# Performance work log

Measured on AMD Instinct MI355X. Metric: run time of the kernel, lower is better.

## Reference

```python
import jax, jax.numpy as jnp
import numpy as np

Q_PTS = jnp.array([0.0, 0.25, 0.5, 0.75, 1.0], dtype=jnp.float32)
LN_EPS = 1e-5


def _lower_median(s):
    # torch.median returns the LOWER of the two middle values for even n
    return s[..., (s.shape[-1] - 1) // 2]


def _quantile_sorted(s, q):
    # torch.quantile default 'linear' interpolation, computed on pre-sorted s
    n = s.shape[-1]
    idx = q * (n - 1)
    lo = jnp.floor(idx).astype(jnp.int32)
    hi = jnp.ceil(idx).astype(jnp.int32)
    frac = (idx - lo).astype(s.dtype)
    return jnp.take(s, lo, axis=-1) * (1.0 - frac) + jnp.take(s, hi, axis=-1) * frac


def _robust_stats(flat):
    # flat: [L-1, B, N] -> [L-1, B, 7]  (median, MAD, 5 quantiles)
    s = jnp.sort(flat, axis=-1)
    med = _lower_median(s)[..., None]
    mad = _lower_median(jnp.sort(jnp.abs(flat - med), axis=-1))[..., None]
    q = _quantile_sorted(s, Q_PTS)
    return jnp.concatenate([med, mad, q], axis=-1)


def _layer_norm(x, eps=LN_EPS):
    mu = x.mean(-1, keepdims=True)
    var = ((x - mu) ** 2).mean(-1, keepdims=True)
    return (x - mu) * jax.lax.rsqrt(var + eps)


def _forward(ws, bs, fc1_w, fc1_b, ln_w, ln_b, gate_w, gate_b, fco_w, fco_b, scale):
    Lm1, B = ws.shape[0], ws.shape[1]
    w_flat = ws.reshape(Lm1, B, -1)
    b_flat = bs.reshape(Lm1, B, -1)
    w_feats = _robust_stats(w_flat)            # [L-1, B, 7]
    b_feats = _robust_stats(b_flat)            # [L-1, B, 7]
    g_mean = w_flat.mean(-1, keepdims=True)    # [L-1, B, 1]
    g_mad = jnp.zeros_like(g_mean)             # MAD over a size-1 axis is exactly 0
    combined = jnp.concatenate([w_feats, b_feats, g_mean, g_mad], axis=-1)  # [L-1, B, 16]
    x = _layer_norm(combined)                  # F.layer_norm without affine
    # ResidualMLP (vectorized over the layer axis l)
    h = jnp.einsum('lbi,lhi->lbh', x, fc1_w) + fc1_b[:, None, :]
    h = _layer_norm(h) * ln_w[:, None, :] + ln_b[:, None, :]
    h = jax.nn.gelu(h, approximate=False)      # nn.GELU() default = exact erf
    gate = jax.nn.sigmoid(jnp.einsum('lbh,lgh->lbg', h, gate_w) + gate_b[:, None, :])
    raw = jnp.einsum('lbg,log->lbo', h * gate, fco_w) + fco_b[:, None, :]
    return jnp.sin(raw) * scale[:, None, None] + 1.0   # [L-1, B, out_dim]


def setup_inputs() -> dict:
    key = jax.random.key(0)
    ks = jax.random.split(key, 8)
    Lm1, B, D, H, F_IN = 3, 64, 512, 64, 16
    return {
        'ws': jax.random.normal(ks[0], (Lm1, B, D, D), jnp.float32) * 0.05,
        'bs': jax.random.normal(ks[1], (Lm1, B, D), jnp.float32) * 0.05,
        'w_last': jax.random.normal(ks[2], (B, D, D), jnp.float32) * 0.05,
        'b_last': jax.random.normal(ks[3], (B, D), jnp.float32) * 0.05,
        'fc1_w': jax.random.normal(ks[4], (Lm1, H, F_IN), jnp.float32) * 0.2,
        'fc1_b': jnp.zeros((Lm1, H), jnp.float32),
        'ln_w': jnp.ones((Lm1, H), jnp.float32),
        'ln_b': jnp.zeros((Lm1, H), jnp.float32),
        'gate_w': jax.random.normal(ks[5], (Lm1, H, H), jnp.float32) * 0.15,
        'gate_b': jnp.zeros((Lm1, H), jnp.float32),
        'fco_w': jax.random.normal(ks[6], (Lm1, D, H), jnp.float32) * 0.1,
        'fco_b': jnp.zeros((Lm1, D), jnp.float32),
        'scale': jnp.full((Lm1,), 0.1, jnp.float32),
    }


def reference(ws, bs, w_last, b_last, fc1_w, fc1_b, ln_w, ln_b, gate_w, gate_b, fco_w, fco_b, scale):
    # w_last / b_last correspond to wsfeat[L-1]: received by forward but never used
    # (loop breaks at i == L-1), matching the torch module exactly.
    return _forward(ws, bs, fc1_w, fc1_b, ln_w, ln_b, gate_w, gate_b, fco_w, fco_b, scale)
```

## Files before the change

kernel.cpp:

```cpp
#include <hip/hip_runtime.h>
#include <cstdint>

#define NROW 192
#define NW   262144
#define NW4  65536
#define NT   1024
#define QCAP 1024
#define MCAP 6144

__device__ __forceinline__ uint32_t mono(float x) {
    uint32_t u = __float_as_uint(x);
    return (u & 0x80000000u) ? ~u : (u | 0x80000000u);
}
__device__ __forceinline__ float unmono(uint32_t u) {
    uint32_t v = (u & 0x80000000u) ? (u & 0x7FFFFFFFu) : ~u;
    return __uint_as_float(v);
}
__device__ __forceinline__ int binof(float x, float lo, float s) {
    float d = (x - lo) * s;
    d = fminf(fmaxf(d, 0.0f), 4095.0f);
    return (int)d;
}

__device__ void block_select(const uint32_t* hist, int nb, uint32_t rank,
                             uint32_t* sbuf, volatile uint32_t* out, int tid) {
    int per = (nb + NT - 1) / NT;
    int base = tid * per;
    uint32_t s = 0;
    for (int i = 0; i < per; ++i) { int idx = base + i; if (idx < nb) s += hist[idx]; }
    uint32_t p = s;
    int lane = tid & 63;
    #pragma unroll
    for (int off = 1; off < 64; off <<= 1) {
        uint32_t v = __shfl_up(p, off);
        if (lane >= off) p += v;
    }
    int w = tid >> 6;
    if (lane == 63) sbuf[w] = p;
    __syncthreads();
    if (tid == 0) {
        uint32_t acc = 0;
        for (int i = 0; i < 16; ++i) { uint32_t t = sbuf[i]; sbuf[16 + i] = acc; acc += t; }
    }
    __syncthreads();
    uint32_t excl = sbuf[16 + w] + p - s;
    if (rank >= excl && rank < excl + s) {
        uint32_t rem = rank - excl;
        for (int i = 0; i < per; ++i) {
            int idx = base + i;
            if (idx >= nb) break;
            uint32_t c = hist[idx];
            if (rem < c) { out[0] = (uint32_t)idx; out[1] = rem; break; }
            rem -= c;
        }
    }
    __syncthreads();
}

__device__ uint32_t seg_select(const uint32_t* seg, uint32_t cnt, uint32_t rank,
                               uint32_t* hist2, uint32_t* sbuf,
                               volatile uint32_t* out2, int tid) {
    for (int i = tid; i < 2048; i += NT) hist2[i] = 0;
    __syncthreads();
    for (uint32_t i = tid; i < cnt; i += NT) atomicAdd(&hist2[seg[i] >> 21], 1u);
    __syncthreads();
    block_select(hist2, 2048, rank, sbuf, out2, tid);
    uint32_t b1 = out2[0], r1 = out2[1];
    __syncthreads();
    for (int i = tid; i < 2048; i += NT) hist2[i] = 0;
    __syncthreads();
    for (uint32_t i = tid; i < cnt; i += NT) {
        uint32_t k = seg[i];
        if ((k >> 21) == b1) atomicAdd(&hist2[(k >> 10) & 2047u], 1u);
    }
    __syncthreads();
    block_select(hist2, 2048, r1, sbuf, out2, tid);
    uint32_t b2 = out2[0], r2 = out2[1];
    __syncthreads();
    for (int i = tid; i < 1024; i += NT) hist2[i] = 0;
    __syncthreads();
    for (uint32_t i = tid; i < cnt; i += NT) {
        uint32_t k = seg[i];
        if ((k >> 21) == b1 && ((k >> 10) & 2047u) == b2)
            atomicAdd(&hist2[k & 1023u], 1u);
    }
    __syncthreads();
    block_select(hist2, 1024, r2, sbuf, out2, tid);
    uint32_t b3 = out2[0];
    __syncthreads();
    return (b1 << 21) + (b2 << 10) + b3;
}

__device__ uint32_t refine_global(const float4* p4, float med, int mode,
                                  uint32_t b1, uint32_t rem,
                                  uint32_t* hist2, uint32_t* sbuf,
                                  volatile uint32_t* out2, int tid) {
    for (int i = tid; i < 2048; i += NT) hist2[i] = 0;
    __syncthreads();
    for (int it = 0; it < 64; ++it) {
        float4 v = p4[tid + it * NT];
        float xs[4] = {v.x, v.y, v.z, v.w};
        #pragma unroll
        for (int c = 0; c < 4; ++c) {
            uint32_t u = mode ? __float_as_uint(fabsf(xs[c] - med)) : mono(xs[c]);
            if ((u >> 20) == b1) atomicAdd(&hist2[(u >> 9) & 2047u], 1u);
        }
    }
    __syncthreads();
    block_select(hist2, 2048, rem, sbuf, out2, tid);
    uint32_t b2 = out2[0], r2 = out2[1];
    __syncthreads();
    for (int i = tid; i < 512; i += NT) hist2[i] = 0;
    __syncthreads();
    for (int it = 0; it < 64; ++it) {
        float4 v = p4[tid + it * NT];
        float xs[4] = {v.x, v.y, v.z, v.w};
        #pragma unroll
        for (int c = 0; c < 4; ++c) {
            uint32_t u = mode ? __float_as_uint(fabsf(xs[c] - med)) : mono(xs[c]);
            if ((u >> 20) == b1 && ((u >> 9) & 2047u) == b2)
                atomicAdd(&hist2[u & 511u], 1u);
        }
    }
    __syncthreads();
    block_select(hist2, 512, r2, sbuf, out2, tid);
    uint32_t b3 = out2[0];
    __syncthreads();
    return (b1 << 20) + (b2 << 9) + b3;
}

__device__ void fb_path(const float4* p4, float* feat, int row,
                        uint32_t* hist, uint32_t* hist2, uint32_t* sbuf,
                        volatile uint32_t* out2, int tid) {
    const uint32_t RANK6[6] = {65535u, 65536u, 131071u, 131072u, 196607u, 196608u};
    for (int i = tid; i < 4096; i += NT) hist[i] = 0;
    __syncthreads();
    for (int it = 0; it < 64; ++it) {
        float4 v = p4[tid + it * NT];
        float xs[4] = {v.x, v.y, v.z, v.w};
        #pragma unroll
        for (int c = 0; c < 4; ++c) atomicAdd(&hist[mono(xs[c]) >> 20], 1u);
    }
    __syncthreads();
    uint32_t bins[6], rems[6];
    for (int k = 0; k < 6; ++k) {
        block_select(hist, 4096, RANK6[k], sbuf, out2, tid);
        bins[k] = out2[0]; rems[k] = out2[1];
        __syncthreads();
    }
    float svv[6];
    for (int k = 0; k < 6; ++k)
        svv[k] = unmono(refine_global(p4, 0.f, 0, bins[k], rems[k], hist2, sbuf, out2, tid));
    if (tid == 0) {
        float* f = feat + row * 16;
        f[0] = svv[2];
        f[3] = 0.25f * svv[0] + 0.75f * svv[1];
        f[4] = 0.5f  * (svv[2] + svv[3]);
        f[5] = 0.75f * svv[4] + 0.25f * svv[5];
    }
    float med = svv[2];
    __syncthreads();
    for (int i = tid; i < 4096; i += NT) hist[i] = 0;
    __syncthreads();
    for (int it = 0; it < 64; ++it) {
        float4 v = p4[tid + it * NT];
        float xs[4] = {v.x, v.y, v.z, v.w};
        #pragma unroll
        for (int c = 0; c < 4; ++c)
            atomicAdd(&hist[__float_as_uint(fabsf(xs[c] - med)) >> 20], 1u);
    }
    __syncthreads();
    block_select(hist, 4096, 131071u, sbuf, out2, tid);
    uint32_t mb = out2[0], mr = out2[1];
    __syncthreads();
    uint32_t mu = refine_global(p4, med, 1, mb, mr, hist2, sbuf, out2, tid);
    if (tid == 0) feat[row * 16 + 1] = __uint_as_float(mu);
}

__global__ __launch_bounds__(NT) void wstats_kernel(const float* __restrict__ wsrc,
                                                    float* __restrict__ feat) {
    const int row = blockIdx.x;
    const int tid = threadIdx.x;
    const float4* __restrict__ p4 = (const float4*)(wsrc + (size_t)row * NW);

    __shared__ uint32_t hist[4096];
    __shared__ uint32_t hist2[2048];
    __shared__ uint32_t sbuf[1024];
    __shared__ uint32_t segs[MCAP];
    __shared__ uint32_t ctrl[48];
    __shared__ float fctrl[8];
    volatile uint32_t* out2 = (volatile uint32_t*)(ctrl + 40);

    const int lane = tid & 63, w = tid >> 6;
    float* fsb = (float*)sbuf;

    {
        float smin = 1e30f, smax = -1e30f;
        #pragma unroll
        for (int k = 0; k < 8; ++k) {
            float4 v = p4[tid + k * NT];
            smin = fminf(smin, fminf(fminf(v.x, v.y), fminf(v.z, v.w)));
            smax = fmaxf(smax, fmaxf(fmaxf(v.x, v.y), fmaxf(v.z, v.w)));
        }
        #pragma unroll
        for (int off = 32; off > 0; off >>= 1) {
            smin = fminf(smin, __shfl_down(smin, off));
            smax = fmaxf(smax, __shfl_down(smax, off));
        }
        if (lane == 0) { fsb[w * 2] = smin; fsb[w * 2 + 1] = smax; }
        __syncthreads();
        if (tid == 0) {
            float mn = 1e30f, mx = -1e30f;
            for (int i = 0; i < 16; ++i) { mn = fminf(mn, fsb[i * 2]); mx = fmaxf(mx, fsb[i * 2 + 1]); }
            float span = mx - mn;
            float lo = mn - 0.0625f * span;
            float s = (span > 0.f) ? 4096.0f / (span * 1.125f) : 0.0f;
            fctrl[0] = lo; fctrl[1] = s;
        }
        __syncthreads();
    }
    const float blo = fctrl[0], bsc = fctrl[1];

    for (int i = tid; i < 4096; i += NT) hist[i] = 0;
    __syncthreads();
    {
        float sum = 0.f, fmn = 1e30f, fmx = -1e30f;
        for (int it = 0; it < 64; it += 8) {
            float4 a[8];
            #pragma unroll
            for (int j = 0; j < 8; ++j) a[j] = p4[tid + (it + j) * NT];
            #pragma unroll
            for (int j = 0; j < 8; ++j) {
                float xs[4] = {a[j].x, a[j].y, a[j].z, a[j].w};
                #pragma unroll
                for (int c = 0; c < 4; ++c) {
                    float x = xs[c];
                    sum += x;
                    fmn = fminf(fmn, x);
                    fmx = fmaxf(fmx, x);
                    atomicAdd(&hist[binof(x, blo, bsc)], 1u);
                }
            }
        }
        #pragma unroll
        for (int off = 32; off > 0; off >>= 1) {
            sum += __shfl_down(sum, off);
            fmn = fminf(fmn, __shfl_down(fmn, off));
            fmx = fmaxf(fmx, __shfl_down(fmx, off));
        }
        __syncthreads();
        if (lane == 0) { fsb[w * 4] = sum; fsb[w * 4 + 1] = fmn; fsb[w * 4 + 2] = fmx; }
        __syncthreads();
        if (tid == 0) { float s = 0; for (int i = 0; i < 16; ++i) s += fsb[i * 4]; feat[row * 16 + 14] = s * (1.0f / (float)NW); }
        if (tid == 1) { float m = 1e30f;  for (int i = 0; i < 16; ++i) m = fminf(m, fsb[i * 4 + 1]); feat[row * 16 + 2] = m; fctrl[2] = m; }
        if (tid == 2) { float M = -1e30f; for (int i = 0; i < 16; ++i) M = fmaxf(M, fsb[i * 4 + 2]); feat[row * 16 + 6] = M; fctrl[3] = M; }
        if (tid == 3) feat[row * 16 + 15] = 0.0f;
        __syncthreads();
    }

    const uint32_t RANKS[6] = {65535u, 65536u, 131071u, 131072u, 196607u, 196608u};
    for (int k = 0; k < 6; ++k) {
        block_select(hist, 4096, RANKS[k], sbuf, out2, tid);
        if (tid == 0) { ctrl[12 + k] = out2[0]; ctrl[18 + k] = out2[1]; }
        __syncthreads();
    }
    if (tid == 0) {
        uint32_t nd = 0;
        for (int k = 0; k < 6; ++k) {
            uint32_t b = ctrl[12 + k];
            int j = -1;
            for (uint32_t t = 0; t < nd; ++t) if (ctrl[24 + t] == b) { j = (int)t; break; }
            if (j < 0) { j = (int)nd; ctrl[24 + nd] = b; nd++; }
            ctrl[32 + k] = (uint32_t)j;
        }
        ctrl[10] = nd; ctrl[11] = 0;
        for (int j = 0; j < 6; ++j) ctrl[j] = 0;
    }
    __syncthreads();
    const uint32_t nd = ctrl[10];
    sbuf[tid] = 0; sbuf[tid + (4096 - NT) ? 0 : 0] = sbuf[tid];
    __syncthreads();
    if (tid < (int)nd) ((uint8_t*)sbuf)[ctrl[24 + tid]] = (uint8_t)(tid + 1);
    __syncthreads();

    {
        const uint8_t* tbl = (const uint8_t*)sbuf;
        for (int it = 0; it < 64; it += 8) {
            float4 a[8];
            #pragma unroll
            for (int j = 0; j < 8; ++j) a[j] = p4[tid + (it + j) * NT];
            #pragma unroll
            for (int j = 0; j < 8; ++j) {
                float xs[4] = {a[j].x, a[j].y, a[j].z, a[j].w};
                #pragma unroll
                for (int c = 0; c < 4; ++c) {
                    float x = xs[c];
                    uint32_t m = tbl[binof(x, blo, bsc)];
                    if (m) {
                        uint32_t jj = m - 1;
                        uint32_t pos = atomicAdd(&ctrl[jj], 1u);
                        if (pos < QCAP) segs[jj * QCAP + pos] = mono(x);
                    }
                }
            }
        }
    }
    __syncthreads();
    if (tid == 0) {
        uint32_t fail = 0;
        for (uint32_t j = 0; j < nd; ++j)
            if (ctrl[j] > QCAP || ctrl[j] != hist[ctrl[24 + j]]) fail = 1;
        ctrl[11] = fail;
    }
    __syncthreads();
    if (ctrl[11]) { fb_path(p4, feat, row, hist, hist2, sbuf, out2, tid); return; }

    float sv[6];
    for (int k = 0; k < 6; ++k) {
        uint32_t j = ctrl[32 + k];
        sv[k] = unmono(seg_select(segs + j * QCAP, ctrl[j], ctrl[18 + k],
                                  hist2, sbuf, out2, tid));
    }
    const float med = sv[2];
    if (tid == 0) {
        float* f = feat + row * 16;
        f[0] = med;
        f[3] = 0.25f * sv[0] + 0.75f * sv[1];
        f[4] = 0.5f  * (sv[2] + sv[3]);
        f[5] = 0.75f * sv[4] + 0.25f * sv[5];
    }

    const float tmax = fmaxf(fctrl[3] - med, med - fctrl[2]);
    const float tsc = (tmax > 0.f) ? 4096.0f / tmax : 0.0f;
    for (int i = tid; i < 4096; i += NT) hist[i] = 0;
    __syncthreads();
    for (int it = 0; it < 64; it += 8) {
        float4 a[8];
        #pragma unroll
        for (int j = 0; j < 8; ++j) a[j] = p4[tid + (it + j) * NT];
        #pragma unroll
        for (int j = 0; j < 8; ++j) {
            float xs[4] = {a[j].x, a[j].y, a[j].z, a[j].w};
            #pragma unroll
            for (int c = 0; c < 4; ++c)
                atomicAdd(&hist[binof(fabsf(xs[c] - med), 0.0f, tsc)], 1u);
        }
    }
    __syncthreads();
    block_select(hist, 4096, 131071u, sbuf, out2, tid);
    const uint32_t mbin = out2[0], mrem = out2[1];
    if (tid == 0) ctrl[8] = 0;
    __syncthreads();

    for (int it = 0; it < 64; it += 8) {
        float4 a[8];
        #pragma unroll
        for (int j = 0; j < 8; ++j) a[j] = p4[tid + (it + j) * NT];
        #pragma unroll
        for (int j = 0; j < 8; ++j) {
            float xs[4] = {a[j].x, a[j].y, a[j].z, a[j].w};
            #pragma unroll
            for (int c = 0; c < 4; ++c) {
                float t = fabsf(xs[c] - med);
                if (binof(t, 0.0f, tsc) == (int)mbin) {
                    uint32_t pos = atomicAdd(&ctrl[8], 1u);
                    if (pos < MCAP) segs[pos] = __float_as_uint(t);
                }
            }
        }
    }
    __syncthreads();
    if (tid == 0) ctrl[11] = (ctrl[8] > MCAP || ctrl[8] != hist[mbin]) ? 1u : 0u;
    __syncthreads();
    if (ctrl[11]) { fb_path(p4, feat, row, hist, hist2, sbuf, out2, tid); return; }
    uint32_t madu = seg_select(segs, ctrl[8], mrem, hist2, sbuf, out2, tid);
    if (tid == 0) feat[row * 16 + 1] = __uint_as_float(madu);
}

__device__ void bitonic512(float* a, int tid) {
    for (int k = 2; k <= 512; k <<= 1) {
        for (int j = k >> 1; j > 0; j >>= 1) {
            __syncthreads();
            for (int i = tid; i < 512; i += 256) {
                int ixj = i ^ j;
                if (ixj > i) {
                    float x = a[i], y = a[ixj];
                    bool up = ((i & k) == 0);
                    if ((x > y) == up) { a[i] = y; a[ixj] = x; }
                }
            }
        }
    }
    __syncthreads();
}

__global__ __launch_bounds__(256) void tail_kernel(
    const float* __restrict__ bsrc, const float* __restrict__ feat,
    const float* __restrict__ fc1_w, const float* __restrict__ fc1_b,
    const float* __restrict__ ln_w,  const float* __restrict__ ln_b,
    const float* __restrict__ gate_w, const float* __restrict__ gate_b,
    const float* __restrict__ fco_w,  const float* __restrict__ fco_b,
    const float* __restrict__ scale,  float* __restrict__ out) {
    const int row = blockIdx.x;
    const int tid = threadIdx.x;
    const int l = row >> 6;
    __shared__ float a[512], d[512];
    __shared__ float x[16], h[64], hg[64], stats[2];

    if (tid < 7)       x[tid] = feat[row * 16 + tid];
    else if (tid == 7) x[14]  = feat[row * 16 + 14];
    else if (tid == 8) x[15]  = 0.0f;

    const float* p = bsrc + (size_t)row * 512;
    for (int i = tid; i < 512; i += 256) a[i] = p[i];
    bitonic512(a, tid);
    const float bmed = a[255];
    if (tid == 0) {
        x[7]  = bmed;
        x[9]  = a[0];
        x[10] = 0.25f * a[127] + 0.75f * a[128];
        x[11] = 0.5f  * (a[255] + a[256]);
        x[12] = 0.75f * a[383] + 0.25f * a[384];
        x[13] = a[511];
    }
    __syncthreads();
    for (int i = tid; i < 512; i += 256) d[i] = fabsf(a[i] - bmed);
    bitonic512(d, tid);
    if (tid == 0) x[8] = d[255];
    __syncthreads();

    if (tid == 0) {
        float mu = 0.f;
        for (int i = 0; i < 16; ++i) mu += x[i];
        mu *= (1.f / 16.f);
        float var = 0.f;
        for (int i = 0; i < 16; ++i) { float dd = x[i] - mu; var += dd * dd; }
        var *= (1.f / 16.f);
        stats[0] = mu; stats[1] = rsqrtf(var + 1e-5f);
    }
    __syncthreads();
    if (tid < 16) x[tid] = (x[tid] - stats[0]) * stats[1];
    __syncthreads();
    if (tid < 64) {
        const float* wv = fc1_w + ((size_t)l * 64 + tid) * 16;
        float acc = fc1_b[l * 64 + tid];
        #pragma unroll
        for (int i = 0; i < 16; ++i) acc += x[i] * wv[i];
        h[tid] = acc;
    }
    __syncthreads();
    if (tid == 0) {
        float mu = 0.f;
        for (int i = 0; i < 64; ++i) mu += h[i];
        mu *= (1.f / 64.f);
        float var = 0.f;
        for (int i = 0; i < 64; ++i) { float dd = h[i] - mu; var += dd * dd; }
        var *= (1.f / 64.f);
        stats[0] = mu; stats[1] = rsqrtf(var + 1e-5f);
    }
    __syncthreads();
    if (tid < 64) {
        float v = (h[tid] - stats[0]) * stats[1] * ln_w[l * 64 + tid] + ln_b[l * 64 + tid];
        h[tid] = 0.5f * v * (1.0f + erff(v * 0.70710678118654752f));
    }
    __syncthreads();
    if (tid < 64) {
        const float* wv = gate_w + ((size_t)l * 64 + tid) * 64;
        float acc = gate_b[l * 64 + tid];
        #pragma unroll
        for (int i = 0; i < 64; ++i) acc += h[i] * wv[i];
        float g = 1.0f / (1.0f + expf(-acc));
        hg[tid] = h[tid] * g;
    }
    __syncthreads();
    const float sc = scale[l];
    for (int o = tid; o < 512; o += 256) {
        const float* wv = fco_w + ((size_t)l * 512 + o) * 64;
        float acc = fco_b[l * 512 + o];
        #pragma unroll
        for (int i = 0; i < 64; ++i) acc += hg[i] * wv[i];
        out[(size_t)row * 512 + o] = sinf(acc) * sc + 1.0f;
    }
}

extern "C" void kernel_launch(void* const* d_in, const int* in_sizes, int n_in,
                              void* d_out, int out_size, void* d_ws, size_t ws_size,
                              hipStream_t stream) {
    const float* ws_in  = (const float*)d_in[0];
    const float* bs_in  = (const float*)d_in[1];
    const float* fc1_w  = (const float*)d_in[4];
    const float* fc1_b  = (const float*)d_in[5];
    const float* ln_w   = (const float*)d_in[6];
    const float* ln_b   = (const float*)d_in[7];
    const float* gate_w = (const float*)d_in[8];
    const float* gate_b = (const float*)d_in[9];
    const float* fco_w  = (const float*)d_in[10];
    const float* fco_b  = (const float*)d_in[11];
    const float* scale  = (const float*)d_in[12];
    float* out  = (float*)d_out;
    float* feat = (float*)d_ws;

    hipLaunchKernelGGL(wstats_kernel, dim3(NROW), dim3(NT), 0, stream, ws_in, feat);
    hipLaunchKernelGGL(tail_kernel, dim3(NROW), dim3(256), 0, stream,
                       bs_in, feat, fc1_w, fc1_b, ln_w, ln_b, gate_w, gate_b,
                       fco_w, fco_b, scale, out);
}
```

Measured before the change: 459.2 us.

## Predict MAD window from histogram to fuse passes and merge bias stats

Computes prefix sums of the coarse histogram so all six quantile bins are found in a single scan. The histogram is also used to bound the MAD bracket around the median before the median is known, so quantile candidates and MAD candidates are gathered in one shared data pass. This removes the separate MAD histogram and collection passes over the 1 MB rows. Exact selection inside each candidate segment now uses brute-force rank counting instead of three-level radix histograms. The bias-vector sorts move out of the MLP kernel into extra blocks of the stats kernel. The cost is O(n²) rank counting on candidate sets and several new failure checks that fall back to the slow path.

```diff
diff --git a/kernel.cpp b/kernel.cpp
--- a/kernel.cpp
+++ b/kernel.cpp
@@ -3,10 +3,9 @@
 
 #define NROW 192
 #define NW   262144
-#define NW4  65536
 #define NT   1024
 #define QCAP 1024
-#define MCAP 6144
+#define SEGS_CAP 8192
 
 __device__ __forceinline__ uint32_t mono(float x) {
     uint32_t u = __float_as_uint(x);
@@ -57,40 +56,6 @@
     __syncthreads();
 }
 
-__device__ uint32_t seg_select(const uint32_t* seg, uint32_t cnt, uint32_t rank,
-                               uint32_t* hist2, uint32_t* sbuf,
-                               volatile uint32_t* out2, int tid) {
-    for (int i = tid; i < 2048; i += NT) hist2[i] = 0;
-    __syncthreads();
-    for (uint32_t i = tid; i < cnt; i += NT) atomicAdd(&hist2[seg[i] >> 21], 1u);
-    __syncthreads();
-    block_select(hist2, 2048, rank, sbuf, out2, tid);
-    uint32_t b1 = out2[0], r1 = out2[1];
-    __syncthreads();
-    for (int i = tid; i < 2048; i += NT) hist2[i] = 0;
-    __syncthreads();
-    for (uint32_t i = tid; i < cnt; i += NT) {
-        uint32_t k = seg[i];
-        if ((k >> 21) == b1) atomicAdd(&hist2[(k >> 10) & 2047u], 1u);
-    }
-    __syncthreads();
-    block_select(hist2, 2048, r1, sbuf, out2, tid);
-    uint32_t b2 = out2[0], r2 = out2[1];
-    __syncthreads();
-    for (int i = tid; i < 1024; i += NT) hist2[i] = 0;
-    __syncthreads();
-    for (uint32_t i = tid; i < cnt; i += NT) {
-        uint32_t k = seg[i];
-        if ((k >> 21) == b1 && ((k >> 10) & 2047u) == b2)
-            atomicAdd(&hist2[k & 1023u], 1u);
-    }
-    __syncthreads();
-    block_select(hist2, 1024, r2, sbuf, out2, tid);
-    uint32_t b3 = out2[0];
-    __syncthreads();
-    return (b1 << 21) + (b2 << 10) + b3;
-}
-
 __device__ uint32_t refine_global(const float4* p4, float med, int mode,
                                   uint32_t b1, uint32_t rem,
                                   uint32_t* hist2, uint32_t* sbuf,
@@ -177,22 +142,81 @@
     if (tid == 0) feat[row * 16 + 1] = __uint_as_float(mu);
 }
 
-__global__ __launch_bounds__(NT) void wstats_kernel(const float* __restrict__ wsrc,
-                                                    float* __restrict__ feat) {
+__device__ __forceinline__ uint32_t Pv(const uint32_t* P, int k) {
+    return (k >= 4096) ? (uint32_t)NW : P[k];
+}
+__device__ __forceinline__ uint32_t wup(float mL, float mR, float tau,
+                                        float blo, float bsc, const uint32_t* P) {
+    const int bR = binof(mR + tau, blo, bsc);
+    const int bL = binof(mL - tau, blo, bsc);
+    return Pv(P, bR + 1) - P[bL];
+}
+__device__ __forceinline__ uint32_t wlow(float mL, float mR, float tau,
+                                         float blo, float bsc, const uint32_t* P) {
+    const int bR = binof(mL + tau, blo, bsc);
+    const int bL = binof(mR - tau, blo, bsc);
+    const uint32_t a = P[bR];
+    const uint32_t b = Pv(P, bL + 1);
+    return (a > b) ? (a - b) : 0u;
+}
+
+__device__ void bitonic512g(float* a, int t2) {
+    for (int k = 2; k <= 512; k <<= 1) {
+        for (int j = k >> 1; j > 0; j >>= 1) {
+            __syncthreads();
+            for (int i = t2; i < 512; i += 256) {
+                int ixj = i ^ j;
+                if (ixj > i) {
+                    float x = a[i], y = a[ixj];
+                    bool up = ((i & k) == 0);
+                    if ((x > y) == up) { a[i] = y; a[ixj] = x; }
+                }
+            }
+        }
+    }
+    __syncthreads();
+}
+
+__global__ __launch_bounds__(NT) void stats_kernel(const float* __restrict__ wsrc,
+                                                   const float* __restrict__ bsrc,
+                                                   float* __restrict__ feat) {
+    const int tid = threadIdx.x;
+    __shared__ uint32_t hist[4096];
+    __shared__ uint32_t sbuf[1024];
+    __shared__ uint32_t segs[SEGS_CAP];
+    __shared__ uint32_t ctrl[64];
+    __shared__ float fctrl[8];
+
+    if (blockIdx.x >= NROW) {
+        const int g = tid >> 8, t2 = tid & 255;
+        const int brow = (blockIdx.x - NROW) * 4 + g;
+        float* a = ((float*)segs) + g * 512;
+        float* d = ((float*)segs) + 2048 + g * 512;
+        const float* p = bsrc + (size_t)brow * 512;
+        for (int i = t2; i < 512; i += 256) a[i] = p[i];
+        bitonic512g(a, t2);
+        const float bmed = a[255];
+        if (t2 == 0) {
+            float* f = feat + brow * 16;
+            f[7]  = bmed;
+            f[9]  = a[0];
+            f[10] = 0.25f * a[127] + 0.75f * a[128];
+            f[11] = 0.5f  * (a[255] + a[256]);
+            f[12] = 0.75f * a[383] + 0.25f * a[384];
+            f[13] = a[511];
+        }
+        __syncthreads();
+        for (int i = t2; i < 512; i += 256) d[i] = fabsf(a[i] - bmed);
+        bitonic512g(d, t2);
+        if (t2 == 0) feat[brow * 16 + 8] = d[255];
+        return;
+    }
+
     const int row = blockIdx.x;
-    const int tid = threadIdx.x;
     const float4* __restrict__ p4 = (const float4*)(wsrc + (size_t)row * NW);
-
-    __shared__ uint32_t hist[4096];
-    __shared__ uint32_t hist2[2048];
-    __shared__ uint32_t sbuf[1024];
-    __shared__ uint32_t segs[MCAP];
-    __shared__ uint32_t ctrl[48];
-    __shared__ float fctrl[8];
-    volatile uint32_t* out2 = (volatile uint32_t*)(ctrl + 40);
-
-    const int lane = tid & 63, w = tid >> 6;
+    const int lane = tid & 63, wv = tid >> 6;
     float* fsb = (float*)sbuf;
+    volatile uint32_t* out2 = (volatile uint32_t*)(ctrl + 62);
 
     {
         float smin = 1e30f, smax = -1e30f;
@@ -207,7 +231,7 @@
             smin = fminf(smin, __shfl_down(smin, off));
             smax = fmaxf(smax, __shfl_down(smax, off));
         }
-        if (lane == 0) { fsb[w * 2] = smin; fsb[w * 2 + 1] = smax; }
+        if (lane == 0) { fsb[wv * 2] = smin; fsb[wv * 2 + 1] = smax; }
         __syncthreads();
         if (tid == 0) {
             float mn = 1e30f, mx = -1e30f;
@@ -226,12 +250,12 @@
     {
         float sum = 0.f, fmn = 1e30f, fmx = -1e30f;
         for (int it = 0; it < 64; it += 8) {
-            float4 a[8];
+            float4 a8[8];
             #pragma unroll
-            for (int j = 0; j < 8; ++j) a[j] = p4[tid + (it + j) * NT];
+            for (int j = 0; j < 8; ++j) a8[j] = p4[tid + (it + j) * NT];
             #pragma unroll
             for (int j = 0; j < 8; ++j) {
-                float xs[4] = {a[j].x, a[j].y, a[j].z, a[j].w};
+                float xs[4] = {a8[j].x, a8[j].y, a8[j].z, a8[j].w};
                 #pragma unroll
                 for (int c = 0; c < 4; ++c) {
                     float x = xs[c];
@@ -249,7 +273,7 @@
             fmx = fmaxf(fmx, __shfl_down(fmx, off));
         }
         __syncthreads();
-        if (lane == 0) { fsb[w * 4] = sum; fsb[w * 4 + 1] = fmn; fsb[w * 4 + 2] = fmx; }
+        if (lane == 0) { fsb[wv * 4] = sum; fsb[wv * 4 + 1] = fmn; fsb[wv * 4 + 2] = fmx; }
         __syncthreads();
         if (tid == 0) { float s = 0; for (int i = 0; i < 16; ++i) s += fsb[i * 4]; feat[row * 16 + 14] = s * (1.0f / (float)NW); }
         if (tid == 1) { float m = 1e30f;  for (int i = 0; i < 16; ++i) m = fminf(m, fsb[i * 4 + 1]); feat[row * 16 + 2] = m; fctrl[2] = m; }
@@ -258,144 +282,249 @@
         __syncthreads();
     }
 
-    const uint32_t RANKS[6] = {65535u, 65536u, 131071u, 131072u, 196607u, 196608u};
-    for (int k = 0; k < 6; ++k) {
-        block_select(hist, 4096, RANKS[k], sbuf, out2, tid);
-        if (tid == 0) { ctrl[12 + k] = out2[0]; ctrl[18 + k] = out2[1]; }
-        __syncthreads();
-    }
-    if (tid == 0) {
-        uint32_t nd = 0;
-        for (int k = 0; k < 6; ++k) {
-            uint32_t b = ctrl[12 + k];
-            int j = -1;
-            for (uint32_t t = 0; t < nd; ++t) if (ctrl[24 + t] == b) { j = (int)t; break; }
-            if (j < 0) { j = (int)nd; ctrl[24 + nd] = b; nd++; }
-            ctrl[32 + k] = (uint32_t)j;
-        }
-        ctrl[10] = nd; ctrl[11] = 0;
+    {
+        const int b4 = tid * 4;
+        const uint32_t v0 = hist[b4], v1 = hist[b4 + 1], v2 = hist[b4 + 2], v3 = hist[b4 + 3];
+        const uint32_t s = v0 + v1 + v2 + v3;
+        uint32_t p = s;
+        #pragma unroll
+        for (int off = 1; off < 64; off <<= 1) {
+            uint32_t t = __shfl_up(p, off);
+            if (lane >= off) p += t;
+        }
+        if (lane == 63) sbuf[wv] = p;
+        __syncthreads();
+        if (tid == 0) {
+            uint32_t acc = 0;
+            for (int i = 0; i < 16; ++i) { uint32_t t = sbuf[i]; sbuf[16 + i] = acc; acc += t; }
+        }
+        __syncthreads();
+        const uint32_t excl = sbuf[16 + wv] + p - s;
+        uint32_t ppA[5];
+        ppA[0] = excl; ppA[1] = excl + v0; ppA[2] = ppA[1] + v1; ppA[3] = ppA[2] + v2; ppA[4] = ppA[3] + v3;
+        hist[b4] = ppA[0]; hist[b4 + 1] = ppA[1]; hist[b4 + 2] = ppA[2]; hist[b4 + 3] = ppA[3];
+        const uint32_t RANKS[6] = {65535u, 65536u, 131071u, 131072u, 196607u, 196608u};
+        #pragma unroll
+        for (int c = 0; c < 4; ++c) {
+            #pragma unroll
+            for (int q = 0; q < 6; ++q) {
+                const uint32_t r = RANKS[q];
+                if (ppA[c] <= r && r < ppA[c + 1]) {
+                    ctrl[12 + q] = (uint32_t)(b4 + c);
+                    ctrl[18 + q] = r - ppA[c];
+                    ctrl[48 + q] = ppA[c + 1] - ppA[c];
+                }
+            }
+        }
+        __syncthreads();
+    }
+
+    if (tid == 0) {
+        uint32_t ndl = 0, fail = 0;
+        #pragma unroll
+        for (int q = 0; q < 6; ++q) {
+            const uint32_t b = ctrl[12 + q];
+            int jf = -1;
+            for (uint32_t t = 0; t < ndl; ++t) if (ctrl[24 + t] == b) { jf = (int)t; break; }
+            if (jf < 0) {
+                jf = (int)ndl;
+                ctrl[24 + ndl] = b;
+                ctrl[30 + ndl] = ctrl[48 + q];
+                ndl++;
+            }
+            ctrl[36 + q] = (uint32_t)jf;
+        }
+        uint32_t off = 0;
+        for (uint32_t t = 0; t < ndl; ++t) {
+            ctrl[54 + t] = off;
+            if (ctrl[30 + t] > QCAP) fail = 1;
+            off += ctrl[30 + t];
+        }
+        if (off > 6144u) fail = 1;
+        if (ctrl[14] == 0u || ctrl[14] == 4095u) fail = 1;
+        ctrl[60] = off;
+        ctrl[10] = ndl;
+        ctrl[11] = fail;
+        #pragma unroll
         for (int j = 0; j < 6; ++j) ctrl[j] = 0;
-    }
-    __syncthreads();
-    const uint32_t nd = ctrl[10];
-    sbuf[tid] = 0; sbuf[tid + (4096 - NT) ? 0 : 0] = sbuf[tid];
-    __syncthreads();
-    if (tid < (int)nd) ((uint8_t*)sbuf)[ctrl[24 + tid]] = (uint8_t)(tid + 1);
-    __syncthreads();
-
+        ctrl[6] = 0;
+        ctrl[7] = 0;
+        ctrl[8] = 0;
+        ctrl[9] = 0;
+        ctrl[48] = 0xFFFFFFFFu; ctrl[49] = 0xFFFFFFFFu;
+    }
+    __syncthreads();
+    if (ctrl[11]) { fb_path(p4, feat, row, hist, segs, sbuf, out2, tid); return; }
+
+    const float wbin = 1.0f / bsc;
+    const uint32_t m0 = ctrl[14];
+
+    sbuf[tid] = 0;
+    {
+        const float mLf = blo + (float)m0 * wbin;
+        const float mRf = mLf + wbin;
+        #pragma unroll
+        for (int c = 0; c < 4; ++c) {
+            const int j = tid * 4 + c;
+            const float tau = (float)j * wbin;
+            const uint32_t up_j = wup(mLf, mRf, tau, blo, bsc, hist);
+            if (up_j <= 131071u) {
+                bool bnd = (j == 4095);
+                if (!bnd) bnd = (wup(mLf, mRf, (float)(j + 1) * wbin, blo, bsc, hist) > 131071u);
+                if (bnd) ctrl[48] = (uint32_t)j;
+            }
+            const uint32_t lo_j = wlow(mLf, mRf, tau, blo, bsc, hist);
+            if (lo_j >= 131072u) {
+                bool bnd = (j == 0);
+                if (!bnd) bnd = (wlow(mLf, mRf, (float)(j - 1) * wbin, blo, bsc, hist) < 131072u);
+                if (bnd) ctrl[49] = (uint32_t)j;
+            }
+        }
+    }
+    __syncthreads();
+    if (tid < (int)ctrl[10]) ((uint8_t*)sbuf)[ctrl[24 + tid]] = (uint8_t)(tid + 1);
+    const uint32_t jlo = ctrl[48], jhi = ctrl[49];
+    float Awin = (jlo == 0xFFFFFFFFu) ? -1.0f : (float)jlo * wbin;
+    float Bwin = (jhi == 0xFFFFFFFFu) ? 3.0e38f : (float)jhi * wbin;
+    Bwin = fmaxf(Bwin, Awin + 3.0f * wbin);
+    const float mtld = blo + ((float)m0 + 0.5f) * wbin;
+    const uint32_t madbase = ctrl[60];
+    __syncthreads();
+
+    uint32_t myclo = 0;
     {
         const uint8_t* tbl = (const uint8_t*)sbuf;
         for (int it = 0; it < 64; it += 8) {
-            float4 a[8];
+            float4 a8[8];
             #pragma unroll
-            for (int j = 0; j < 8; ++j) a[j] = p4[tid + (it + j) * NT];
+            for (int j = 0; j < 8; ++j) a8[j] = p4[tid + (it + j) * NT];
             #pragma unroll
             for (int j = 0; j < 8; ++j) {
-                float xs[4] = {a[j].x, a[j].y, a[j].z, a[j].w};
+                float xs[4] = {a8[j].x, a8[j].y, a8[j].z, a8[j].w};
                 #pragma unroll
                 for (int c = 0; c < 4; ++c) {
                     float x = xs[c];
                     uint32_t m = tbl[binof(x, blo, bsc)];
                     if (m) {
-                        uint32_t jj = m - 1;
+                        uint32_t jj = m - 1u;
                         uint32_t pos = atomicAdd(&ctrl[jj], 1u);
-                        if (pos < QCAP) segs[jj * QCAP + pos] = mono(x);
+                        if (pos < ctrl[30 + jj]) segs[ctrl[54 + jj] + pos] = mono(x);
+                    }
+                    float u = fabsf(x - mtld);
+                    if (u <= Awin) myclo++;
+                    else if (u <= Bwin) {
+                        uint32_t pos = atomicAdd(&ctrl[6], 1u);
+                        uint32_t slot = madbase + pos;
+                        if (slot < SEGS_CAP) segs[slot] = __float_as_uint(x);
                     }
                 }
             }
         }
     }
     __syncthreads();
-    if (tid == 0) {
+    #pragma unroll
+    for (int off = 32; off > 0; off >>= 1) myclo += __shfl_down(myclo, off);
+    if (lane == 0) sbuf[wv] = myclo;
+    __syncthreads();
+    if (tid == 0) {
+        uint32_t clo = 0;
+        for (int i = 0; i < 16; ++i) clo += sbuf[i];
+        ctrl[7] = clo;
         uint32_t fail = 0;
-        for (uint32_t j = 0; j < nd; ++j)
-            if (ctrl[j] > QCAP || ctrl[j] != hist[ctrl[24 + j]]) fail = 1;
+        const uint32_t ndl = ctrl[10];
+        for (uint32_t j = 0; j < ndl; ++j) if (ctrl[j] != ctrl[30 + j]) fail = 1;
+        if (ctrl[6] > SEGS_CAP - madbase) fail = 1;
         ctrl[11] = fail;
     }
     __syncthreads();
-    if (ctrl[11]) { fb_path(p4, feat, row, hist, hist2, sbuf, out2, tid); return; }
-
-    float sv[6];
-    for (int k = 0; k < 6; ++k) {
-        uint32_t j = ctrl[32 + k];
-        sv[k] = unmono(seg_select(segs + j * QCAP, ctrl[j], ctrl[18 + k],
-                                  hist2, sbuf, out2, tid));
-    }
-    const float med = sv[2];
+    if (ctrl[11]) { fb_path(p4, feat, row, hist, segs, sbuf, out2, tid); return; }
+
+    {
+        const uint32_t ndl = ctrl[10];
+        for (uint32_t j = 0; j < ndl; ++j) {
+            const uint32_t cnt = ctrl[j];
+            const uint32_t base = ctrl[54 + j];
+            if ((uint32_t)tid < cnt) {
+                const uint32_t key = segs[base + tid];
+                uint32_t r = 0;
+                for (uint32_t i = 0; i < cnt; ++i) {
+                    const uint32_t ki = segs[base + i];
+                    r += (ki < key || (ki == key && i < (uint32_t)tid)) ? 1u : 0u;
+                }
+                #pragma unroll
+                for (int q = 0; q < 6; ++q)
+                    if (ctrl[36 + q] == j && ctrl[18 + q] == r) ctrl[42 + q] = key;
+            }
+        }
+    }
+    __syncthreads();
+    const float med = unmono(ctrl[44]);
     if (tid == 0) {
         float* f = feat + row * 16;
         f[0] = med;
-        f[3] = 0.25f * sv[0] + 0.75f * sv[1];
-        f[4] = 0.5f  * (sv[2] + sv[3]);
-        f[5] = 0.75f * sv[4] + 0.25f * sv[5];
-    }
-
-    const float tmax = fmaxf(fctrl[3] - med, med - fctrl[2]);
-    const float tsc = (tmax > 0.f) ? 4096.0f / tmax : 0.0f;
-    for (int i = tid; i < 4096; i += NT) hist[i] = 0;
-    __syncthreads();
-    for (int it = 0; it < 64; it += 8) {
-        float4 a[8];
-        #pragma unroll
-        for (int j = 0; j < 8; ++j) a[j] = p4[tid + (it + j) * NT];
-        #pragma unroll
-        for (int j = 0; j < 8; ++j) {
-            float xs[4] = {a[j].x, a[j].y, a[j].z, a[j].w};
+        f[3] = 0.25f * unmono(ctrl[42]) + 0.75f * unmono(ctrl[43]);
+        f[4] = 0.5f  * (med + unmono(ctrl[45]));
+        f[5] = 0.75f * unmono(ctrl[46]) + 0.25f * unmono(ctrl[47]);
+    }
+
+    const uint32_t mcnt = ctrl[6];
+    const float thq = Awin + wbin;
+    const float tcq = Bwin - 2.0f * wbin;
+    float tk[8];
+    uint32_t rr[8];
+    uint32_t n2t = 0, n2c = 0;
+    #pragma unroll
+    for (int q = 0; q < 8; ++q) {
+        const uint32_t i = (uint32_t)tid + (uint32_t)q * NT;
+        float t = 3.0e38f;
+        if (i < mcnt) {
+            float x = __uint_as_float(segs[madbase + i]);
+            t = fabsf(x - med);
+            segs[madbase + i] = __float_as_uint(t);
+            n2t += (t <= thq) ? 1u : 0u;
+            n2c += (t <= tcq) ? 1u : 0u;
+        }
+        tk[q] = t;
+        rr[q] = 0;
+    }
+    #pragma unroll
+    for (int off = 32; off > 0; off >>= 1) {
+        n2t += __shfl_down(n2t, off);
+        n2c += __shfl_down(n2c, off);
+    }
+    if (lane == 0) { atomicAdd(&ctrl[8], n2t); atomicAdd(&ctrl[9], n2c); }
+    __syncthreads();
+    if (tid == 0) {
+        const uint32_t clo = ctrl[7];
+        uint32_t fail = 0;
+        if (clo > 131071u) fail = 1;
+        if (clo + ctrl[8] > 131071u) fail = 1;
+        if (clo + ctrl[9] < 131072u) fail = 1;
+        if (!fail && (131071u - clo) >= mcnt) fail = 1;
+        ctrl[11] = fail;
+    }
+    __syncthreads();
+    if (ctrl[11]) { fb_path(p4, feat, row, hist, segs, sbuf, out2, tid); return; }
+    const uint32_t kR = 131071u - ctrl[7];
+    if ((uint32_t)tid < mcnt) {
+        for (uint32_t jj = 0; jj < mcnt; ++jj) {
+            const float tj = __uint_as_float(segs[madbase + jj]);
             #pragma unroll
-            for (int c = 0; c < 4; ++c)
-                atomicAdd(&hist[binof(fabsf(xs[c] - med), 0.0f, tsc)], 1u);
-        }
-    }
-    __syncthreads();
-    block_select(hist, 4096, 131071u, sbuf, out2, tid);
-    const uint32_t mbin = out2[0], mrem = out2[1];
-    if (tid == 0) ctrl[8] = 0;
-    __syncthreads();
-
-    for (int it = 0; it < 64; it += 8) {
-        float4 a[8];
-        #pragma unroll
-        for (int j = 0; j < 8; ++j) a[j] = p4[tid + (it + j) * NT];
-        #pragma unroll
-        for (int j = 0; j < 8; ++j) {
-            float xs[4] = {a[j].x, a[j].y, a[j].z, a[j].w};
-            #pragma unroll
-            for (int c = 0; c < 4; ++c) {
-                float t = fabsf(xs[c] - med);
-                if (binof(t, 0.0f, tsc) == (int)mbin) {
-                    uint32_t pos = atomicAdd(&ctrl[8], 1u);
-                    if (pos < MCAP) segs[pos] = __float_as_uint(t);
-                }
-            }
-        }
-    }
-    __syncthreads();
-    if (tid == 0) ctrl[11] = (ctrl[8] > MCAP || ctrl[8] != hist[mbin]) ? 1u : 0u;
-    __syncthreads();
-    if (ctrl[11]) { fb_path(p4, feat, row, hist, hist2, sbuf, out2, tid); return; }
-    uint32_t madu = seg_select(segs, ctrl[8], mrem, hist2, sbuf, out2, tid);
-    if (tid == 0) feat[row * 16 + 1] = __uint_as_float(madu);
-}
-
-__device__ void bitonic512(float* a, int tid) {
-    for (int k = 2; k <= 512; k <<= 1) {
-        for (int j = k >> 1; j > 0; j >>= 1) {
-            __syncthreads();
-            for (int i = tid; i < 512; i += 256) {
-                int ixj = i ^ j;
-                if (ixj > i) {
-                    float x = a[i], y = a[ixj];
-                    bool up = ((i & k) == 0);
-                    if ((x > y) == up) { a[i] = y; a[ixj] = x; }
-                }
-            }
-        }
-    }
-    __syncthreads();
-}
-
-__global__ __launch_bounds__(256) void tail_kernel(
-    const float* __restrict__ bsrc, const float* __restrict__ feat,
+            for (int q = 0; q < 8; ++q) {
+                const uint32_t idx = (uint32_t)tid + (uint32_t)q * NT;
+                rr[q] += (tj < tk[q] || (tj == tk[q] && jj < idx)) ? 1u : 0u;
+            }
+        }
+        #pragma unroll
+        for (int q = 0; q < 8; ++q) {
+            const uint32_t idx = (uint32_t)tid + (uint32_t)q * NT;
+            if (idx < mcnt && rr[q] == kR) feat[row * 16 + 1] = tk[q];
+        }
+    }
+}
+
+__global__ __launch_bounds__(256) void mlp_kernel(
+    const float* __restrict__ feat,
     const float* __restrict__ fc1_w, const float* __restrict__ fc1_b,
     const float* __restrict__ ln_w,  const float* __restrict__ ln_b,
     const float* __restrict__ gate_w, const float* __restrict__ gate_b,
@@ -404,29 +533,9 @@
     const int row = blockIdx.x;
     const int tid = threadIdx.x;
     const int l = row >> 6;
-    __shared__ float a[512], d[512];
     __shared__ float x[16], h[64], hg[64], stats[2];
 
-    if (tid < 7)       x[tid] = feat[row * 16 + tid];
-    else if (tid == 7) x[14]  = feat[row * 16 + 14];
-    else if (tid == 8) x[15]  = 0.0f;
-
-    const float* p = bsrc + (size_t)row * 512;
-    for (int i = tid; i < 512; i += 256) a[i] = p[i];
-    bitonic512(a, tid);
-    const float bmed = a[255];
-    if (tid == 0) {
-        x[7]  = bmed;
-        x[9]  = a[0];
-        x[10] = 0.25f * a[127] + 0.75f * a[128];
-        x[11] = 0.5f  * (a[255] + a[256]);
-        x[12] = 0.75f * a[383] + 0.25f * a[384];
-        x[13] = a[511];
-    }
-    __syncthreads();
-    for (int i = tid; i < 512; i += 256) d[i] = fabsf(a[i] - bmed);
-    bitonic512(d, tid);
-    if (tid == 0) x[8] = d[255];
+    if (tid < 16) x[tid] = feat[row * 16 + tid];
     __syncthreads();
 
     if (tid == 0) {
@@ -500,8 +609,9 @@
     float* out  = (float*)d_out;
     float* feat = (float*)d_ws;
 
-    hipLaunchKernelGGL(wstats_kernel, dim3(NROW), dim3(NT), 0, stream, ws_in, feat);
-    hipLaunchKernelGGL(tail_kernel, dim3(NROW), dim3(256), 0, stream,
-                       bs_in, feat, fc1_w, fc1_b, ln_w, ln_b, gate_w, gate_b,
+    hipLaunchKernelGGL(stats_kernel, dim3(NROW + NROW / 4), dim3(NT), 0, stream,
+                       ws_in, bs_in, feat);
+    hipLaunchKernelGGL(mlp_kernel, dim3(NROW), dim3(256), 0, stream,
+                       feat, fc1_w, fc1_b, ln_w, ln_b, gate_w, gate_b,
                        fco_w, fco_b, scale, out);
 }
```

Result: slower. 928.1 us (+102.1%).
